# Performance work log

Hardware: AMD Instinct MI355X
Metric: run time of the kernel (lower is better)

## Reference

```python
import jax, jax.numpy as jnp
import numpy as np

HEAD_DIM = 32
N_HEADS = 4
C = HEAD_DIM * N_HEADS  # 128
N = 256
LN_EPS = 1e-5


def setup_inputs() -> dict:
    key = jax.random.key(0)
    ks = jax.random.split(key, 8)
    s = 1.0 / np.sqrt(C)
    return {
        "x": jax.random.normal(ks[0], (1, N, N, C), dtype=jnp.float32),
        "w_ln": jnp.ones((C,), dtype=jnp.float32),
        "b_ln": jnp.zeros((C,), dtype=jnp.float32),
        "w_b": jax.random.normal(ks[1], (N_HEADS, C), dtype=jnp.float32) * s,
        "w_q": jax.random.normal(ks[2], (C, C), dtype=jnp.float32) * s,
        "w_k": jax.random.normal(ks[3], (C, C), dtype=jnp.float32) * s,
        "w_v": jax.random.normal(ks[4], (C, C), dtype=jnp.float32) * s,
        "w_g": jax.random.normal(ks[5], (C, C), dtype=jnp.float32) * s,
        "w_o": jax.random.normal(ks[6], (C, C), dtype=jnp.float32) * s,
    }


def reference(x, w_ln, b_ln, w_b, w_q, w_k, w_v, w_g, w_o):
    # x: [1, N, N, C]; ending=False -> no permute
    xs = x[0]  # [N, N, C]
    # LayerNorm over last dim
    mu = jnp.mean(xs, axis=-1, keepdims=True)
    var = jnp.mean(jnp.square(xs - mu), axis=-1, keepdims=True)
    h = (xs - mu) * jax.lax.rsqrt(var + LN_EPS) * w_ln + b_ln  # [N, N, C]

    # pair bias: [N, N, h] -> [h, N, N]
    bias = jnp.einsum("ijc,hc->hij", h, w_b)

    # q/k/v: linear (weight stored [out, in], applied as x @ W^T), split heads
    q = jnp.einsum("bkc,oc->bko", h, w_q).reshape(N, N, N_HEADS, HEAD_DIM)
    k = jnp.einsum("bkc,oc->bko", h, w_k).reshape(N, N, N_HEADS, HEAD_DIM)
    v = jnp.einsum("bkc,oc->bko", h, w_v).reshape(N, N, N_HEADS, HEAD_DIM)

    scale = HEAD_DIM ** -0.5
    # scores: [N(b), h, N(q), N(k)], bias broadcast over row-batch b
    a = jnp.einsum("bqhd,bkhd->bhqk", q, k) * scale + bias[None]
    p = jax.nn.softmax(a, axis=-1)
    o = jnp.einsum("bhqk,bkhd->bqhd", p, v).reshape(N, N, C)

    g = jax.nn.sigmoid(jnp.einsum("bkc,oc->bko", h, w_g))
    out = jnp.einsum("bkc,oc->bko", o * g, w_o)  # [N, N, C]
    return out[None]  # [1, N, N, C]
```

## Files before the change

kernel.cpp:

```cpp
#include <hip/hip_runtime.h>

typedef short bf16x8 __attribute__((ext_vector_type(8)));
typedef ushort u16x4 __attribute__((ext_vector_type(4)));
typedef float f32x4 __attribute__((ext_vector_type(4)));

__device__ __forceinline__ ushort f2b(float f) {
    uint u = __builtin_bit_cast(uint, f);
    uint r = (u + 0x7fffu + ((u >> 16) & 1u)) >> 16;
    return (ushort)r;
}
__device__ __forceinline__ float b2f(ushort s) {
    uint u = ((uint)s) << 16;
    return __builtin_bit_cast(float, u);
}
__device__ __forceinline__ uint cvt_pk(float a, float b) {
    uint r;
    asm("v_cvt_pk_bf16_f32 %0, %1, %2" : "=v"(r) : "v"(a), "v"(b));
    return r;
}

__global__ __launch_bounds__(128) void prep_kernel(
        const float* __restrict__ w_q, const float* __restrict__ w_k,
        const float* __restrict__ w_v, const float* __restrict__ w_g,
        const float* __restrict__ w_o,
        ushort* __restrict__ wall, ushort* __restrict__ wo) {
    int row = blockIdx.x, col = threadIdx.x;
    int cs = col ^ ((row & 7) << 3);
    if (row < 512) {
        float val;
        if (row < 128)      val = w_q[row * 128 + col];
        else if (row < 256) val = w_k[(row - 128) * 128 + col];
        else if (row < 384) val = w_v[(row - 256) * 128 + col];
        else                val = w_g[(row - 384) * 128 + col];
        wall[row * 128 + cs] = f2b(val);
    } else {
        int r = row - 512;
        wo[r * 128 + cs] = f2b(w_o[r * 128 + col]);
    }
}

__global__ __launch_bounds__(256) void ln_bias_kernel(
        const float* __restrict__ x, const float* __restrict__ w_ln,
        const float* __restrict__ b_ln, const float* __restrict__ w_b,
        ushort* __restrict__ h, float* __restrict__ biasT) {
    int row = blockIdx.x * 4 + (threadIdx.x >> 6);
    int lane = threadIdx.x & 63;
    float2 v = reinterpret_cast<const float2*>(x + (size_t)row * 128)[lane];
    float s = v.x + v.y;
    float sq = v.x * v.x + v.y * v.y;
#pragma unroll
    for (int off = 32; off >= 1; off >>= 1) {
        s += __shfl_xor(s, off);
        sq += __shfl_xor(sq, off);
    }
    float mean = s * (1.0f / 128.0f);
    float var = sq * (1.0f / 128.0f) - mean * mean;
    float rstd = rsqrtf(var + 1e-5f);
    int c0 = lane * 2;
    float h0 = (v.x - mean) * rstd * w_ln[c0] + b_ln[c0];
    float h1 = (v.y - mean) * rstd * w_ln[c0 + 1] + b_ln[c0 + 1];
    ushort2 o;
    o.x = f2b(h0);
    o.y = f2b(h1);
    reinterpret_cast<ushort2*>(h + (size_t)row * 128)[lane ^ ((row & 7) << 2)] = o;
    float p0 = h0 * w_b[c0]       + h1 * w_b[c0 + 1];
    float p1 = h0 * w_b[128 + c0] + h1 * w_b[128 + c0 + 1];
    float p2 = h0 * w_b[256 + c0] + h1 * w_b[256 + c0 + 1];
    float p3 = h0 * w_b[384 + c0] + h1 * w_b[384 + c0 + 1];
#pragma unroll
    for (int off = 32; off >= 1; off >>= 1) {
        p0 += __shfl_xor(p0, off);
        p1 += __shfl_xor(p1, off);
        p2 += __shfl_xor(p2, off);
        p3 += __shfl_xor(p3, off);
    }
    if (lane < 4) {
        float val = (lane == 0) ? p0 : (lane == 1) ? p1 : (lane == 2) ? p2 : p3;
        biasT[(size_t)lane * 65536 + (size_t)(row & 255) * 256 + (row >> 8)] = val;
    }
}

__global__ __launch_bounds__(256) void proj_kernel(
        const ushort* __restrict__ h, const ushort* __restrict__ wall,
        ushort* __restrict__ qp, ushort* __restrict__ kp,
        ushort* __restrict__ vt, ushort* __restrict__ g) {
    __shared__ ushort walls[16384];
    int m0 = blockIdx.x * 64;
    int tid = threadIdx.x, w = tid >> 6, lane = tid & 63;
    int lo = lane & 15, hi = lane >> 4;
    int arow = m0 + w * 16 + lo;
    bf16x8 a[4];
#pragma unroll
    for (int ks = 0; ks < 4; ++ks)
        a[ks] = *(const bf16x8*)(h + (size_t)arow * 128 +
                                 ((ks * 32 + hi * 8) ^ ((arow & 7) << 3)));
    int bb = m0 >> 8;
    int pbm = (m0 & 255) + w * 16 + hi * 4;
    int mrow = m0 + w * 16 + hi * 4;
#pragma unroll 1
    for (int y = 0; y < 4; ++y) {
        __syncthreads();
        for (int idx = tid; idx < 2048; idx += 256)
            ((float4*)walls)[idx] = ((const float4*)(wall + (size_t)y * 16384))[idx];
        __syncthreads();
#pragma unroll
        for (int nt = 0; nt < 8; ++nt) {
            f32x4 acc = {0.f, 0.f, 0.f, 0.f};
            int lr = nt * 16 + lo;
#pragma unroll
            for (int ks = 0; ks < 4; ++ks) {
                bf16x8 bf = *(const bf16x8*)(walls + lr * 128 +
                                             ((ks * 32 + hi * 8) ^ ((lr & 7) << 3)));
                acc = __builtin_amdgcn_mfma_f32_16x16x32_bf16(a[ks], bf, acc, 0, 0, 0);
            }
            int d = nt * 16 + lo, head = d >> 5, dh = d & 31;
            size_t base = ((size_t)(bb * 4 + head)) * 8192;
            if (y == 0) {
#pragma unroll
                for (int r = 0; r < 4; ++r)
                    qp[base + (pbm + r) * 32 + dh] =
                        f2b(acc[r] * 0.17677669529663687f);
            } else if (y == 1) {
#pragma unroll
                for (int r = 0; r < 4; ++r) {
                    int p = pbm + r;
                    int ch = (dh >> 3) ^ ((p >> 1) & 3);
                    kp[base + p * 32 + (ch << 3) + (dh & 7)] = f2b(acc[r]);
                }
            } else if (y == 2) {
                u16x4 t4;
#pragma unroll
                for (int r = 0; r < 4; ++r) t4[r] = f2b(acc[r]);
                *(u16x4*)(vt + base + dh * 256 +
                          ((((pbm >> 3) ^ (dh & 7)) << 3) + (pbm & 7))) = t4;
            } else {
#pragma unroll
                for (int r = 0; r < 4; ++r)
                    g[(size_t)(mrow + r) * 128 + nt * 16 + lo] =
                        f2b(1.0f / (1.0f + __expf(-acc[r])));
            }
        }
    }
}

__global__ __launch_bounds__(256, 4) void attn_kernel(
        const ushort* __restrict__ qp, const ushort* __restrict__ kp,
        const ushort* __restrict__ vt, const ushort* __restrict__ gm,
        const float* __restrict__ biasT, ushort* __restrict__ og) {
    __shared__ ushort Ks[8192];
    __shared__ ushort Vs[8192];
    __shared__ ushort P[4][1024];
    int blk = blockIdx.x, bh = blk & 1023, hf = blk >> 10;
    int b = bh >> 2, head = bh & 3;
    int tid = threadIdx.x, w = tid >> 6, lane = tid & 63;
    int lo = lane & 15, hi = lane >> 4;
    const ushort* kb = kp + (size_t)bh * 8192;
    const ushort* vb = vt + (size_t)bh * 8192;
    for (int idx = tid; idx < 1024; idx += 256) {
        ((float4*)Ks)[idx] = ((const float4*)kb)[idx];
        ((float4*)Vs)[idx] = ((const float4*)vb)[idx];
    }
    __syncthreads();
    ushort* pw = P[w];
    int vsw = (lo & 7);
    int kch = hi ^ ((lo >> 1) & 3);
    int pw0 = lo * 32 + (((hi >> 1) ^ (lo & 3)) << 3) + ((hi & 1) << 2);
    int pw1 = lo * 32 + (((2 | (hi >> 1)) ^ (lo & 3)) << 3) + ((hi & 1) << 2);
    int prd = lo * 32 + ((hi ^ (lo & 3)) << 3);

    int qrow0 = hf * 128 + w * 32 + lo;
    int qrow1 = qrow0 + 16;
    bf16x8 qa0 = *(const bf16x8*)(qp + (size_t)bh * 8192 + qrow0 * 32 + hi * 8);
    bf16x8 qa1 = *(const bf16x8*)(qp + (size_t)bh * 8192 + qrow1 * 32 + hi * 8);
    const float* btq0 = biasT + (size_t)head * 65536 + (size_t)(hi * 4) * 256 + qrow0;
    const float* btq1 = btq0 + 16;
    float l0 = 0.f, l1 = 0.f;
    f32x4 a00 = {0.f, 0.f, 0.f, 0.f}, a01 = {0.f, 0.f, 0.f, 0.f};
    f32x4 a10 = {0.f, 0.f, 0.f, 0.f}, a11 = {0.f, 0.f, 0.f, 0.f};
#pragma unroll
    for (int c = 0; c < 8; ++c) {
        f32x4 c00, c01, c10, c11;
#pragma unroll
        for (int r = 0; r < 4; ++r) {
            c00[r] = btq0[(c * 32 + r) * 256];
            c01[r] = btq0[(c * 32 + 16 + r) * 256];
            c10[r] = btq1[(c * 32 + r) * 256];
            c11[r] = btq1[(c * 32 + 16 + r) * 256];
        }
        bf16x8 kf0 = *(const bf16x8*)(Ks + (c * 32 + lo) * 32 + kch * 8);
        bf16x8 kf1 = *(const bf16x8*)(Ks + (c * 32 + 16 + lo) * 32 + kch * 8);
        f32x4 s00 = __builtin_amdgcn_mfma_f32_16x16x32_bf16(kf0, qa0, c00, 0, 0, 0);
        f32x4 s01 = __builtin_amdgcn_mfma_f32_16x16x32_bf16(kf1, qa0, c01, 0, 0, 0);
        f32x4 s10 = __builtin_amdgcn_mfma_f32_16x16x32_bf16(kf0, qa1, c10, 0, 0, 0);
        f32x4 s11 = __builtin_amdgcn_mfma_f32_16x16x32_bf16(kf1, qa1, c11, 0, 0, 0);
        float e00 = __expf(s00[0]), e01 = __expf(s00[1]),
              e02 = __expf(s00[2]), e03 = __expf(s00[3]);
        float e04 = __expf(s01[0]), e05 = __expf(s01[1]),
              e06 = __expf(s01[2]), e07 = __expf(s01[3]);
        float e10 = __expf(s10[0]), e11 = __expf(s10[1]),
              e12 = __expf(s10[2]), e13 = __expf(s10[3]);
        float e14 = __expf(s11[0]), e15 = __expf(s11[1]),
              e16 = __expf(s11[2]), e17 = __expf(s11[3]);
        l0 += ((e00 + e01) + (e02 + e03)) + ((e04 + e05) + (e06 + e07));
        l1 += ((e10 + e11) + (e12 + e13)) + ((e14 + e15) + (e16 + e17));
        uint2 w00, w01, w10, w11;
        w00.x = cvt_pk(e00, e01); w00.y = cvt_pk(e02, e03);
        w01.x = cvt_pk(e04, e05); w01.y = cvt_pk(e06, e07);
        w10.x = cvt_pk(e10, e11); w10.y = cvt_pk(e12, e13);
        w11.x = cvt_pk(e14, e15); w11.y = cvt_pk(e16, e17);
        *(uint2*)(pw + pw0) = w00;
        *(uint2*)(pw + pw1) = w01;
        *(uint2*)(pw + 512 + pw0) = w10;
        *(uint2*)(pw + 512 + pw1) = w11;
        bf16x8 pf0 = *(const bf16x8*)(pw + prd);
        bf16x8 pf1 = *(const bf16x8*)(pw + 512 + prd);
        bf16x8 v0 = *(const bf16x8*)(Vs + lo * 256 + (((c * 4 + hi) ^ vsw) << 3));
        bf16x8 v1 = *(const bf16x8*)(Vs + (16 + lo) * 256 + (((c * 4 + hi) ^ vsw) << 3));
        a00 = __builtin_amdgcn_mfma_f32_16x16x32_bf16(v0, pf0, a00, 0, 0, 0);
        a01 = __builtin_amdgcn_mfma_f32_16x16x32_bf16(v1, pf0, a01, 0, 0, 0);
        a10 = __builtin_amdgcn_mfma_f32_16x16x32_bf16(v0, pf1, a10, 0, 0, 0);
        a11 = __builtin_amdgcn_mfma_f32_16x16x32_bf16(v1, pf1, a11, 0, 0, 0);
    }
    l0 += __shfl_xor(l0, 16);
    l0 += __shfl_xor(l0, 32);
    l1 += __shfl_xor(l1, 16);
    l1 += __shfl_xor(l1, 32);
    float rl0 = 1.0f / l0, rl1 = 1.0f / l1;
    int e0 = head * 32 + hi * 4, e1 = e0 + 16;
    int sw = (lo & 7) << 3;
    size_t mr0 = (size_t)b * 256 + qrow0;
    size_t mr1 = mr0 + 16;
    u16x4 g00 = *(const u16x4*)(gm + mr0 * 128 + e0);
    u16x4 g01 = *(const u16x4*)(gm + mr0 * 128 + e1);
    u16x4 g10 = *(const u16x4*)(gm + mr1 * 128 + e0);
    u16x4 g11 = *(const u16x4*)(gm + mr1 * 128 + e1);
    u16x4 o00, o01, o10, o11;
#pragma unroll
    for (int r = 0; r < 4; ++r) {
        o00[r] = f2b(a00[r] * rl0 * b2f(g00[r]));
        o01[r] = f2b(a01[r] * rl0 * b2f(g01[r]));
        o10[r] = f2b(a10[r] * rl1 * b2f(g10[r]));
        o11[r] = f2b(a11[r] * rl1 * b2f(g11[r]));
    }
    *(u16x4*)(og + mr0 * 128 + (e0 ^ sw)) = o00;
    *(u16x4*)(og + mr0 * 128 + (e1 ^ sw)) = o01;
    *(u16x4*)(og + mr1 * 128 + (e0 ^ sw)) = o10;
    *(u16x4*)(og + mr1 * 128 + (e1 ^ sw)) = o11;
}

__global__ __launch_bounds__(256) void out_kernel(
        const ushort* __restrict__ og, const ushort* __restrict__ wo,
        float* __restrict__ out) {
    __shared__ ushort wos[16384];
    int m0 = blockIdx.x * 64;
    for (int idx = threadIdx.x; idx < 2048; idx += 256)
        ((float4*)wos)[idx] = ((const float4*)wo)[idx];
    int tid = threadIdx.x, w = tid >> 6, lane = tid & 63;
    int lo = lane & 15, hi = lane >> 4;
    int arow = m0 + w * 16 + lo;
    bf16x8 oa[4];
#pragma unroll
    for (int ks = 0; ks < 4; ++ks)
        oa[ks] = *(const bf16x8*)(og + (size_t)arow * 128 +
                                  ((ks * 32 + hi * 8) ^ ((arow & 7) << 3)));
    __syncthreads();
    int mrow = m0 + w * 16 + hi * 4;
#pragma unroll
    for (int nt = 0; nt < 8; ++nt) {
        f32x4 acc = {0.f, 0.f, 0.f, 0.f};
        int lr = nt * 16 + lo;
#pragma unroll
        for (int ks = 0; ks < 4; ++ks) {
            bf16x8 bf = *(const bf16x8*)(wos + lr * 128 +
                                         ((ks * 32 + hi * 8) ^ ((lr & 7) << 3)));
            acc = __builtin_amdgcn_mfma_f32_16x16x32_bf16(oa[ks], bf, acc, 0, 0, 0);
        }
#pragma unroll
        for (int r = 0; r < 4; ++r)
            out[(size_t)(mrow + r) * 128 + nt * 16 + lo] = acc[r];
    }
}

extern "C" void kernel_launch(void* const* d_in, const int* in_sizes, int n_in,
                              void* d_out, int out_size, void* d_ws, size_t ws_size,
                              hipStream_t stream) {
    const float* x    = (const float*)d_in[0];
    const float* w_ln = (const float*)d_in[1];
    const float* b_ln = (const float*)d_in[2];
    const float* w_b  = (const float*)d_in[3];
    const float* w_q  = (const float*)d_in[4];
    const float* w_k  = (const float*)d_in[5];
    const float* w_v  = (const float*)d_in[6];
    const float* w_g  = (const float*)d_in[7];
    const float* w_o  = (const float*)d_in[8];
    float* out = (float*)d_out;

    char* ws = (char*)d_ws;
    const size_t MB16 = (size_t)65536 * 128 * sizeof(ushort);
    ushort* h      = (ushort*)(ws + 0 * MB16);
    ushort* qp     = (ushort*)(ws + 1 * MB16);
    ushort* kp     = (ushort*)(ws + 2 * MB16);
    ushort* vt     = (ushort*)(ws + 3 * MB16);
    ushort* g      = (ushort*)(ws + 4 * MB16);
    ushort* og     = (ushort*)(ws + 5 * MB16);
    float*  biasT  = (float*)(ws + 6 * MB16);
    ushort* wall   = (ushort*)(ws + 6 * MB16 + (size_t)65536 * 4 * 4);
    ushort* wo     = wall + 512 * 128;

    prep_kernel<<<640, 128, 0, stream>>>(w_q, w_k, w_v, w_g, w_o, wall, wo);
    ln_bias_kernel<<<65536 / 4, 256, 0, stream>>>(x, w_ln, b_ln, w_b, h, biasT);
    proj_kernel<<<1024, 256, 0, stream>>>(h, wall, qp, kp, vt, g);
    attn_kernel<<<2048, 256, 0, stream>>>(qp, kp, vt, g, biasT, og);
    out_kernel<<<1024, 256, 0, stream>>>(og, wo, out);
}
```

Before: 108.2 us.

## Fuse LayerNorm and pair-bias into projection kernel, keep h in shared memory

Merges the LayerNorm/pair-bias kernel into the QKVG projection kernel, so each block normalizes its 64 rows into LDS instead of writing bf16 h to global memory and reading it back. The MFMA operands are swapped for the q/k/g outputs so each lane holds four consecutive output columns and can write them as one 8-byte vector store instead of scattered 2-byte stores. The first weight slice is loaded before the LayerNorm work, which removes one kernel launch and a 16 MB round trip. In exchange the block uses more LDS, which may limit occupancy.

```diff
diff --git a/kernel.cpp b/kernel.cpp
--- a/kernel.cpp
+++ b/kernel.cpp
@@ -39,95 +39,100 @@
     }
 }
 
-__global__ __launch_bounds__(256) void ln_bias_kernel(
+__global__ __launch_bounds__(256, 3) void lnproj_kernel(
         const float* __restrict__ x, const float* __restrict__ w_ln,
         const float* __restrict__ b_ln, const float* __restrict__ w_b,
-        ushort* __restrict__ h, float* __restrict__ biasT) {
-    int row = blockIdx.x * 4 + (threadIdx.x >> 6);
-    int lane = threadIdx.x & 63;
-    float2 v = reinterpret_cast<const float2*>(x + (size_t)row * 128)[lane];
-    float s = v.x + v.y;
-    float sq = v.x * v.x + v.y * v.y;
-#pragma unroll
-    for (int off = 32; off >= 1; off >>= 1) {
-        s += __shfl_xor(s, off);
-        sq += __shfl_xor(sq, off);
-    }
-    float mean = s * (1.0f / 128.0f);
-    float var = sq * (1.0f / 128.0f) - mean * mean;
-    float rstd = rsqrtf(var + 1e-5f);
-    int c0 = lane * 2;
-    float h0 = (v.x - mean) * rstd * w_ln[c0] + b_ln[c0];
-    float h1 = (v.y - mean) * rstd * w_ln[c0 + 1] + b_ln[c0 + 1];
-    ushort2 o;
-    o.x = f2b(h0);
-    o.y = f2b(h1);
-    reinterpret_cast<ushort2*>(h + (size_t)row * 128)[lane ^ ((row & 7) << 2)] = o;
-    float p0 = h0 * w_b[c0]       + h1 * w_b[c0 + 1];
-    float p1 = h0 * w_b[128 + c0] + h1 * w_b[128 + c0 + 1];
-    float p2 = h0 * w_b[256 + c0] + h1 * w_b[256 + c0 + 1];
-    float p3 = h0 * w_b[384 + c0] + h1 * w_b[384 + c0 + 1];
-#pragma unroll
-    for (int off = 32; off >= 1; off >>= 1) {
-        p0 += __shfl_xor(p0, off);
-        p1 += __shfl_xor(p1, off);
-        p2 += __shfl_xor(p2, off);
-        p3 += __shfl_xor(p3, off);
-    }
-    if (lane < 4) {
-        float val = (lane == 0) ? p0 : (lane == 1) ? p1 : (lane == 2) ? p2 : p3;
-        biasT[(size_t)lane * 65536 + (size_t)(row & 255) * 256 + (row >> 8)] = val;
-    }
-}
-
-__global__ __launch_bounds__(256) void proj_kernel(
-        const ushort* __restrict__ h, const ushort* __restrict__ wall,
+        const ushort* __restrict__ wall,
         ushort* __restrict__ qp, ushort* __restrict__ kp,
-        ushort* __restrict__ vt, ushort* __restrict__ g) {
+        ushort* __restrict__ vt, ushort* __restrict__ g,
+        float* __restrict__ biasT) {
+    __shared__ ushort hl[8192];
     __shared__ ushort walls[16384];
     int m0 = blockIdx.x * 64;
     int tid = threadIdx.x, w = tid >> 6, lane = tid & 63;
+
+    for (int idx = tid; idx < 2048; idx += 256)
+        ((float4*)walls)[idx] = ((const float4*)wall)[idx];
+
+    {
+        int rr = lane >> 2, part = lane & 3;
+        int lrow = w * 16 + rr;
+        int grow = m0 + lrow;
+        const float4* xr = (const float4*)(x + (size_t)grow * 128 + part * 32);
+        float4 xv[8];
+        float s = 0.f, sq = 0.f;
+#pragma unroll
+        for (int j = 0; j < 8; ++j) {
+            xv[j] = xr[j];
+            s += (xv[j].x + xv[j].y) + (xv[j].z + xv[j].w);
+            sq += (xv[j].x * xv[j].x + xv[j].y * xv[j].y)
+                + (xv[j].z * xv[j].z + xv[j].w * xv[j].w);
+        }
+        s += __shfl_xor(s, 1);   s += __shfl_xor(s, 2);
+        sq += __shfl_xor(sq, 1); sq += __shfl_xor(sq, 2);
+        float mean = s * (1.0f / 128.0f);
+        float var = sq * (1.0f / 128.0f) - mean * mean;
+        float rstd = rsqrtf(var + 1e-5f);
+        int c0 = part * 32;
+        int swr = (lrow & 7) << 3;
+        float pb[4] = {0.f, 0.f, 0.f, 0.f};
+#pragma unroll
+        for (int j = 0; j < 8; j += 2) {
+            ushort hs[8];
+#pragma unroll
+            for (int jj = 0; jj < 2; ++jj) {
+                float4 xj = xv[j + jj];
+                float4 wl = ((const float4*)(w_ln + c0))[j + jj];
+                float4 bl = ((const float4*)(b_ln + c0))[j + jj];
+                float h0 = (xj.x - mean) * rstd * wl.x + bl.x;
+                float h1 = (xj.y - mean) * rstd * wl.y + bl.y;
+                float h2 = (xj.z - mean) * rstd * wl.z + bl.z;
+                float h3 = (xj.w - mean) * rstd * wl.w + bl.w;
+#pragma unroll
+                for (int hh = 0; hh < 4; ++hh) {
+                    float4 wb4 = ((const float4*)(w_b + hh * 128 + c0))[j + jj];
+                    pb[hh] += (h0 * wb4.x + h1 * wb4.y) + (h2 * wb4.z + h3 * wb4.w);
+                }
+                hs[jj * 4 + 0] = f2b(h0); hs[jj * 4 + 1] = f2b(h1);
+                hs[jj * 4 + 2] = f2b(h2); hs[jj * 4 + 3] = f2b(h3);
+            }
+            int col = c0 + j * 4;
+            *(bf16x8*)(hl + lrow * 128 + (col ^ swr)) = *(const bf16x8*)hs;
+        }
+#pragma unroll
+        for (int hh = 0; hh < 4; ++hh) {
+            pb[hh] += __shfl_xor(pb[hh], 1);
+            pb[hh] += __shfl_xor(pb[hh], 2);
+        }
+        biasT[(size_t)part * 65536 + (size_t)(grow & 255) * 256 + (grow >> 8)] = pb[part];
+    }
+    __syncthreads();
+
     int lo = lane & 15, hi = lane >> 4;
-    int arow = m0 + w * 16 + lo;
+    int arow = w * 16 + lo;
     bf16x8 a[4];
 #pragma unroll
     for (int ks = 0; ks < 4; ++ks)
-        a[ks] = *(const bf16x8*)(h + (size_t)arow * 128 +
+        a[ks] = *(const bf16x8*)(hl + arow * 128 +
                                  ((ks * 32 + hi * 8) ^ ((arow & 7) << 3)));
     int bb = m0 >> 8;
+    int pcol = (m0 & 255) + w * 16 + lo;
     int pbm = (m0 & 255) + w * 16 + hi * 4;
-    int mrow = m0 + w * 16 + hi * 4;
 #pragma unroll 1
     for (int y = 0; y < 4; ++y) {
-        __syncthreads();
-        for (int idx = tid; idx < 2048; idx += 256)
-            ((float4*)walls)[idx] = ((const float4*)(wall + (size_t)y * 16384))[idx];
-        __syncthreads();
 #pragma unroll
         for (int nt = 0; nt < 8; ++nt) {
+            int lr = nt * 16 + lo;
             f32x4 acc = {0.f, 0.f, 0.f, 0.f};
-            int lr = nt * 16 + lo;
-#pragma unroll
-            for (int ks = 0; ks < 4; ++ks) {
-                bf16x8 bf = *(const bf16x8*)(walls + lr * 128 +
-                                             ((ks * 32 + hi * 8) ^ ((lr & 7) << 3)));
-                acc = __builtin_amdgcn_mfma_f32_16x16x32_bf16(a[ks], bf, acc, 0, 0, 0);
-            }
-            int d = nt * 16 + lo, head = d >> 5, dh = d & 31;
-            size_t base = ((size_t)(bb * 4 + head)) * 8192;
-            if (y == 0) {
-#pragma unroll
-                for (int r = 0; r < 4; ++r)
-                    qp[base + (pbm + r) * 32 + dh] =
-                        f2b(acc[r] * 0.17677669529663687f);
-            } else if (y == 1) {
-#pragma unroll
-                for (int r = 0; r < 4; ++r) {
-                    int p = pbm + r;
-                    int ch = (dh >> 3) ^ ((p >> 1) & 3);
-                    kp[base + p * 32 + (ch << 3) + (dh & 7)] = f2b(acc[r]);
+            if (y == 2) {
+#pragma unroll
+                for (int ks = 0; ks < 4; ++ks) {
+                    bf16x8 bf = *(const bf16x8*)(walls + lr * 128 +
+                                                 ((ks * 32 + hi * 8) ^ ((lr & 7) << 3)));
+                    acc = __builtin_amdgcn_mfma_f32_16x16x32_bf16(a[ks], bf, acc, 0, 0, 0);
                 }
-            } else if (y == 2) {
+                int d = nt * 16 + lo, head = d >> 5, dh = d & 31;
+                size_t base = ((size_t)(bb * 4 + head)) * 8192;
                 u16x4 t4;
 #pragma unroll
                 for (int r = 0; r < 4; ++r) t4[r] = f2b(acc[r]);
@@ -135,10 +140,43 @@
                           ((((pbm >> 3) ^ (dh & 7)) << 3) + (pbm & 7))) = t4;
             } else {
 #pragma unroll
-                for (int r = 0; r < 4; ++r)
-                    g[(size_t)(mrow + r) * 128 + nt * 16 + lo] =
-                        f2b(1.0f / (1.0f + __expf(-acc[r])));
+                for (int ks = 0; ks < 4; ++ks) {
+                    bf16x8 bf = *(const bf16x8*)(walls + lr * 128 +
+                                                 ((ks * 32 + hi * 8) ^ ((lr & 7) << 3)));
+                    acc = __builtin_amdgcn_mfma_f32_16x16x32_bf16(bf, a[ks], acc, 0, 0, 0);
+                }
+                if (y == 0) {
+                    int head = nt >> 1;
+                    size_t base = ((size_t)(bb * 4 + head)) * 8192;
+                    u16x4 t4;
+#pragma unroll
+                    for (int r = 0; r < 4; ++r)
+                        t4[r] = f2b(acc[r] * 0.17677669529663687f);
+                    *(u16x4*)(qp + base + pcol * 32 + (nt & 1) * 16 + hi * 4) = t4;
+                } else if (y == 1) {
+                    int head = nt >> 1;
+                    size_t base = ((size_t)(bb * 4 + head)) * 8192;
+                    int ch = ((nt & 1) * 2 + (hi >> 1)) ^ ((pcol >> 1) & 3);
+                    u16x4 t4;
+#pragma unroll
+                    for (int r = 0; r < 4; ++r) t4[r] = f2b(acc[r]);
+                    *(u16x4*)(kp + base + pcol * 32 + ch * 8 + (hi & 1) * 4) = t4;
+                } else {
+                    u16x4 t4;
+#pragma unroll
+                    for (int r = 0; r < 4; ++r)
+                        t4[r] = f2b(1.0f / (1.0f + __expf(-acc[r])));
+                    *(u16x4*)(g + (size_t)(m0 + w * 16 + lo) * 128 +
+                              nt * 16 + hi * 4) = t4;
+                }
             }
+        }
+        if (y < 3) {
+            __syncthreads();
+            for (int idx = tid; idx < 2048; idx += 256)
+                ((float4*)walls)[idx] =
+                    ((const float4*)(wall + (size_t)(y + 1) * 16384))[idx];
+            __syncthreads();
         }
     }
 }
@@ -297,19 +335,18 @@
 
     char* ws = (char*)d_ws;
     const size_t MB16 = (size_t)65536 * 128 * sizeof(ushort);
-    ushort* h      = (ushort*)(ws + 0 * MB16);
-    ushort* qp     = (ushort*)(ws + 1 * MB16);
-    ushort* kp     = (ushort*)(ws + 2 * MB16);
-    ushort* vt     = (ushort*)(ws + 3 * MB16);
-    ushort* g      = (ushort*)(ws + 4 * MB16);
-    ushort* og     = (ushort*)(ws + 5 * MB16);
-    float*  biasT  = (float*)(ws + 6 * MB16);
-    ushort* wall   = (ushort*)(ws + 6 * MB16 + (size_t)65536 * 4 * 4);
+    ushort* qp     = (ushort*)(ws + 0 * MB16);
+    ushort* kp     = (ushort*)(ws + 1 * MB16);
+    ushort* vt     = (ushort*)(ws + 2 * MB16);
+    ushort* g      = (ushort*)(ws + 3 * MB16);
+    ushort* og     = (ushort*)(ws + 4 * MB16);
+    float*  biasT  = (float*)(ws + 5 * MB16);
+    ushort* wall   = (ushort*)(ws + 5 * MB16 + (size_t)65536 * 4 * 4);
     ushort* wo     = wall + 512 * 128;
 
     prep_kernel<<<640, 128, 0, stream>>>(w_q, w_k, w_v, w_g, w_o, wall, wo);
-    ln_bias_kernel<<<65536 / 4, 256, 0, stream>>>(x, w_ln, b_ln, w_b, h, biasT);
-    proj_kernel<<<1024, 256, 0, stream>>>(h, wall, qp, kp, vt, g);
+    lnproj_kernel<<<1024, 256, 0, stream>>>(x, w_ln, b_ln, w_b, wall,
+                                            qp, kp, vt, g, biasT);
     attn_kernel<<<2048, 256, 0, stream>>>(qp, kp, vt, g, biasT, og);
     out_kernel<<<1024, 256, 0, stream>>>(og, wo, out);
 }
```

Result: faster. 99.39 us (-8.2%).

## Double-buffer proj weights via async LDS loads, split grid, vectorize stores

Applied to the files above, without the earlier changes.

The projection kernel now runs a 2D grid where each block handles two of the four weight matrices. Weight tiles are streamed into two LDS slots with global_load_lds, so the load of the next slot overlaps MFMA work on the current one. The q/k/g outputs are computed with swapped MFMA operands so each lane can write 4-element vector stores instead of scattered scalar stores. The attention kernel raises wave priority around MFMA groups with s_setprio. The costs are that the A-fragment loads of h are duplicated across the two grid halves and the hand-written vmcnt wait is fragile.

```diff
diff --git a/kernel.cpp b/kernel.cpp
--- a/kernel.cpp
+++ b/kernel.cpp
@@ -17,6 +17,22 @@
     uint r;
     asm("v_cvt_pk_bf16_f32 %0, %1, %2" : "=v"(r) : "v"(a), "v"(b));
     return r;
+}
+__device__ __forceinline__ void stage16k(const ushort* gsrc, ushort* ldst,
+                                         int w, int lane) {
+#pragma unroll
+    for (int c2 = 0; c2 < 4; ++c2) {
+        int off = (w * 4 + c2) * 512;
+        __builtin_amdgcn_global_load_lds(
+            (const __attribute__((address_space(1))) void*)(gsrc + off + lane * 8),
+            (__attribute__((address_space(3))) void*)(ldst + off),
+            16, 0, 0);
+    }
+}
+__device__ __forceinline__ void stage_barrier() {
+    asm volatile("s_waitcnt lgkmcnt(0) vmcnt(4)" ::: "memory");
+    __builtin_amdgcn_sched_barrier(0);
+    __builtin_amdgcn_s_barrier();
 }
 
 __global__ __launch_bounds__(128) void prep_kernel(
@@ -80,13 +96,19 @@
     }
 }
 
-__global__ __launch_bounds__(256) void proj_kernel(
+__global__ __launch_bounds__(256, 5) void proj_kernel(
         const ushort* __restrict__ h, const ushort* __restrict__ wall,
         ushort* __restrict__ qp, ushort* __restrict__ kp,
         ushort* __restrict__ vt, ushort* __restrict__ g) {
-    __shared__ ushort walls[16384];
+    __shared__ ushort slot0[8192];
+    __shared__ ushort slot1[8192];
     int m0 = blockIdx.x * 64;
+    int yhalf = blockIdx.y;
     int tid = threadIdx.x, w = tid >> 6, lane = tid & 63;
+    const ushort* wsrc = wall + (size_t)yhalf * 32768;
+
+    stage16k(wsrc, slot1, w, lane);
+
     int lo = lane & 15, hi = lane >> 4;
     int arow = m0 + w * 16 + lo;
     bf16x8 a[4];
@@ -94,40 +116,31 @@
     for (int ks = 0; ks < 4; ++ks)
         a[ks] = *(const bf16x8*)(h + (size_t)arow * 128 +
                                  ((ks * 32 + hi * 8) ^ ((arow & 7) << 3)));
+    __syncthreads();
+
     int bb = m0 >> 8;
+    int pcol = (m0 & 255) + w * 16 + lo;
     int pbm = (m0 & 255) + w * 16 + hi * 4;
-    int mrow = m0 + w * 16 + hi * 4;
 #pragma unroll 1
-    for (int y = 0; y < 4; ++y) {
-        __syncthreads();
-        for (int idx = tid; idx < 2048; idx += 256)
-            ((float4*)walls)[idx] = ((const float4*)(wall + (size_t)y * 16384))[idx];
-        __syncthreads();
-#pragma unroll
-        for (int nt = 0; nt < 8; ++nt) {
+    for (int s = 0; s < 4; ++s) {
+        if (s < 3)
+            stage16k(wsrc + (size_t)(s + 1) * 8192, (s & 1) ? slot1 : slot0, w, lane);
+        const ushort* cur = (s & 1) ? slot0 : slot1;
+        int y = yhalf * 2 + (s >> 1);
+#pragma unroll
+        for (int ntl = 0; ntl < 4; ++ntl) {
+            int nt = (s & 1) * 4 + ntl;
+            int lrl = ntl * 16 + lo;
             f32x4 acc = {0.f, 0.f, 0.f, 0.f};
-            int lr = nt * 16 + lo;
-#pragma unroll
-            for (int ks = 0; ks < 4; ++ks) {
-                bf16x8 bf = *(const bf16x8*)(walls + lr * 128 +
-                                             ((ks * 32 + hi * 8) ^ ((lr & 7) << 3)));
-                acc = __builtin_amdgcn_mfma_f32_16x16x32_bf16(a[ks], bf, acc, 0, 0, 0);
-            }
-            int d = nt * 16 + lo, head = d >> 5, dh = d & 31;
-            size_t base = ((size_t)(bb * 4 + head)) * 8192;
-            if (y == 0) {
-#pragma unroll
-                for (int r = 0; r < 4; ++r)
-                    qp[base + (pbm + r) * 32 + dh] =
-                        f2b(acc[r] * 0.17677669529663687f);
-            } else if (y == 1) {
-#pragma unroll
-                for (int r = 0; r < 4; ++r) {
-                    int p = pbm + r;
-                    int ch = (dh >> 3) ^ ((p >> 1) & 3);
-                    kp[base + p * 32 + (ch << 3) + (dh & 7)] = f2b(acc[r]);
+            if (y == 2) {
+#pragma unroll
+                for (int ks = 0; ks < 4; ++ks) {
+                    bf16x8 bf = *(const bf16x8*)(cur + lrl * 128 +
+                                                 ((ks * 32 + hi * 8) ^ ((lrl & 7) << 3)));
+                    acc = __builtin_amdgcn_mfma_f32_16x16x32_bf16(a[ks], bf, acc, 0, 0, 0);
                 }
-            } else if (y == 2) {
+                int d = nt * 16 + lo, head = d >> 5, dh = d & 31;
+                size_t base = ((size_t)(bb * 4 + head)) * 8192;
                 u16x4 t4;
 #pragma unroll
                 for (int r = 0; r < 4; ++r) t4[r] = f2b(acc[r]);
@@ -135,11 +148,38 @@
                           ((((pbm >> 3) ^ (dh & 7)) << 3) + (pbm & 7))) = t4;
             } else {
 #pragma unroll
-                for (int r = 0; r < 4; ++r)
-                    g[(size_t)(mrow + r) * 128 + nt * 16 + lo] =
-                        f2b(1.0f / (1.0f + __expf(-acc[r])));
+                for (int ks = 0; ks < 4; ++ks) {
+                    bf16x8 bf = *(const bf16x8*)(cur + lrl * 128 +
+                                                 ((ks * 32 + hi * 8) ^ ((lrl & 7) << 3)));
+                    acc = __builtin_amdgcn_mfma_f32_16x16x32_bf16(bf, a[ks], acc, 0, 0, 0);
+                }
+                if (y == 0) {
+                    int head = nt >> 1;
+                    size_t base = ((size_t)(bb * 4 + head)) * 8192;
+                    u16x4 t4;
+#pragma unroll
+                    for (int r = 0; r < 4; ++r)
+                        t4[r] = f2b(acc[r] * 0.17677669529663687f);
+                    *(u16x4*)(qp + base + pcol * 32 + (nt & 1) * 16 + hi * 4) = t4;
+                } else if (y == 1) {
+                    int head = nt >> 1;
+                    size_t base = ((size_t)(bb * 4 + head)) * 8192;
+                    int ch = ((nt & 1) * 2 + (hi >> 1)) ^ ((pcol >> 1) & 3);
+                    u16x4 t4;
+#pragma unroll
+                    for (int r = 0; r < 4; ++r) t4[r] = f2b(acc[r]);
+                    *(u16x4*)(kp + base + pcol * 32 + ch * 8 + (hi & 1) * 4) = t4;
+                } else {
+                    u16x4 t4;
+#pragma unroll
+                    for (int r = 0; r < 4; ++r)
+                        t4[r] = f2b(1.0f / (1.0f + __expf(-acc[r])));
+                    *(u16x4*)(g + (size_t)(m0 + w * 16 + lo) * 128 +
+                              nt * 16 + hi * 4) = t4;
+                }
             }
         }
+        stage_barrier();
     }
 }
 
@@ -189,10 +229,12 @@
         }
         bf16x8 kf0 = *(const bf16x8*)(Ks + (c * 32 + lo) * 32 + kch * 8);
         bf16x8 kf1 = *(const bf16x8*)(Ks + (c * 32 + 16 + lo) * 32 + kch * 8);
+        __builtin_amdgcn_s_setprio(1);
         f32x4 s00 = __builtin_amdgcn_mfma_f32_16x16x32_bf16(kf0, qa0, c00, 0, 0, 0);
         f32x4 s01 = __builtin_amdgcn_mfma_f32_16x16x32_bf16(kf1, qa0, c01, 0, 0, 0);
         f32x4 s10 = __builtin_amdgcn_mfma_f32_16x16x32_bf16(kf0, qa1, c10, 0, 0, 0);
         f32x4 s11 = __builtin_amdgcn_mfma_f32_16x16x32_bf16(kf1, qa1, c11, 0, 0, 0);
+        __builtin_amdgcn_s_setprio(0);
         float e00 = __expf(s00[0]), e01 = __expf(s00[1]),
               e02 = __expf(s00[2]), e03 = __expf(s00[3]);
         float e04 = __expf(s01[0]), e05 = __expf(s01[1]),
@@ -216,10 +258,12 @@
         bf16x8 pf1 = *(const bf16x8*)(pw + 512 + prd);
         bf16x8 v0 = *(const bf16x8*)(Vs + lo * 256 + (((c * 4 + hi) ^ vsw) << 3));
         bf16x8 v1 = *(const bf16x8*)(Vs + (16 + lo) * 256 + (((c * 4 + hi) ^ vsw) << 3));
+        __builtin_amdgcn_s_setprio(1);
         a00 = __builtin_amdgcn_mfma_f32_16x16x32_bf16(v0, pf0, a00, 0, 0, 0);
         a01 = __builtin_amdgcn_mfma_f32_16x16x32_bf16(v1, pf0, a01, 0, 0, 0);
         a10 = __builtin_amdgcn_mfma_f32_16x16x32_bf16(v0, pf1, a10, 0, 0, 0);
         a11 = __builtin_amdgcn_mfma_f32_16x16x32_bf16(v1, pf1, a11, 0, 0, 0);
+        __builtin_amdgcn_s_setprio(0);
     }
     l0 += __shfl_xor(l0, 16);
     l0 += __shfl_xor(l0, 32);
@@ -309,7 +353,7 @@
 
     prep_kernel<<<640, 128, 0, stream>>>(w_q, w_k, w_v, w_g, w_o, wall, wo);
     ln_bias_kernel<<<65536 / 4, 256, 0, stream>>>(x, w_ln, b_ln, w_b, h, biasT);
-    proj_kernel<<<1024, 256, 0, stream>>>(h, wall, qp, kp, vt, g);
+    proj_kernel<<<dim3(1024, 2), 256, 0, stream>>>(h, wall, qp, kp, vt, g);
     attn_kernel<<<2048, 256, 0, stream>>>(qp, kp, vt, g, biasT, og);
     out_kernel<<<1024, 256, 0, stream>>>(og, wo, out);
 }
```

Measured after the change: 100.9 us. 1.07x faster.
